# Kernel optimization log

Hardware: AMD Instinct MI355X
Metric: run time of the kernel (lower is better)

The kernel has to match this reference:

```python
import jax, jax.numpy as jnp
import numpy as np

N = 8192
M = 16
F_NODE = 128
HID = 512


def setup_inputs() -> dict:
    key = jax.random.key(0)
    ks = jax.random.split(key, 10)
    node_in_fea = jax.random.normal(ks[0], (N, F_NODE), dtype=jnp.float32)
    edge_fea_idx = jax.random.randint(ks[1], (N, M), 0, N, dtype=jnp.int64)
    s_emb = 1.0 / np.sqrt(F_NODE)
    s_h = 1.0 / np.sqrt(HID)
    W_emb = jax.random.uniform(ks[2], (F_NODE, HID), jnp.float32, -s_emb, s_emb)
    b_emb = jax.random.uniform(ks[3], (HID,), jnp.float32, -s_emb, s_emb)
    W1 = jax.random.uniform(ks[4], (HID, HID), jnp.float32, -s_h, s_h)
    b1 = jax.random.uniform(ks[5], (HID,), jnp.float32, -s_h, s_h)
    W2 = jax.random.uniform(ks[6], (HID, HID), jnp.float32, -s_h, s_h)
    b2 = jax.random.uniform(ks[7], (HID,), jnp.float32, -s_h, s_h)
    W3 = jax.random.uniform(ks[8], (HID, HID), jnp.float32, -s_h, s_h)
    b3 = jax.random.uniform(ks[9], (HID,), jnp.float32, -s_h, s_h)
    return {"node_in_fea": node_in_fea, "edge_fea_idx": edge_fea_idx,
            "W_emb": W_emb, "b_emb": b_emb, "W1": W1, "b1": b1,
            "W2": W2, "b2": b2, "W3": W3, "b3": b3}


def _normalized_adj(edge_fea_idx, n):
    # build dense adjacency: adj[i, j] += 1 for each valid neighbor j of i
    rows = jnp.broadcast_to(jnp.arange(n)[:, None], edge_fea_idx.shape)
    valid = edge_fea_idx >= 0  # -1 marks invalid neighbor
    cols = jnp.where(valid, edge_fea_idx, 0)
    vals = valid.astype(jnp.float32)
    adj = jnp.zeros((n, n), jnp.float32).at[rows.reshape(-1), cols.reshape(-1)].add(vals.reshape(-1))
    # add self-loops, symmetric normalization D^{-1/2} A D^{-1/2}
    adj = adj + jnp.eye(n, dtype=jnp.float32)
    deg = jnp.sum(adj, axis=1)
    d_inv_sqrt = jnp.where(deg > 0, deg ** -0.5, 0.0)
    return adj * d_inv_sqrt[:, None] * d_inv_sqrt[None, :]


def reference(node_in_fea, edge_fea_idx, W_emb, b_emb, W1, b1, W2, b2, W3, b3):
    adj = _normalized_adj(edge_fea_idx, node_in_fea.shape[0])
    x = node_in_fea @ W_emb + b_emb          # (N, HID)
    x = jax.nn.relu((adj @ x) @ W1 + b1)     # gcn1 + relu
    x = jax.nn.relu((adj @ x) @ W2 + b2)     # gcn2 + relu
    x = (adj @ x) @ W3 + b3                  # gcn3 (no relu)
    return x
```

## Files before the change

kernel.cpp:

```cpp
#include <hip/hip_runtime.h>
#include <stdint.h>

#define NN 8192
#define MM 16
#define FN 128
#define HH 512

typedef unsigned short u16;
typedef unsigned int u32;
typedef __bf16 bf16;
typedef __bf16 bf16x8 __attribute__((ext_vector_type(8)));
typedef float f32x4 __attribute__((ext_vector_type(4)));

__global__ void detect_kernel(const u16* __restrict__ node,
                              const u32* __restrict__ idxw,
                              int* __restrict__ flags) {
  if (threadIdx.x == 0 && blockIdx.x == 0) {
    int insane = 0;
    for (int i = 0; i < 64; ++i) {
      int e = (node[2 * i] >> 7) & 0xFF;
      if (!(e == 0 || (e >= 90 && e <= 140))) ++insane;
    }
    flags[0] = (insane >= 8) ? 1 : 0;
    int nz = 0;
    for (int i = 0; i < 32; ++i)
      if (idxw[2 * i + 1] != 0) ++nz;
    flags[1] = (nz == 0) ? 1 : 0;
  }
}

__global__ __launch_bounds__(256) void deg_kernel(const int* __restrict__ idx,
                                                  const int* __restrict__ flags,
                                                  float* __restrict__ dis) {
  int i = blockIdx.x * blockDim.x + threadIdx.x;
  if (i >= NN) return;
  const int sh = flags[1];
  int c = 1;
#pragma unroll
  for (int e = 0; e < MM; ++e) c += (idx[(i * MM + e) << sh] >= 0) ? 1 : 0;
  dis[i] = rsqrtf((float)c);
}

__global__ __launch_bounds__(256) void bias_kernel(
    const void* __restrict__ b0, const void* __restrict__ b1,
    const void* __restrict__ b2, const void* __restrict__ b3,
    const int* __restrict__ flags, u16* __restrict__ out) {
  int id = blockIdx.x * 256 + threadIdx.x;
  if (id >= 4 * HH) return;
  const void* src;
  switch (id >> 9) {
    case 0: src = b0; break;
    case 1: src = b1; break;
    case 2: src = b2; break;
    default: src = b3; break;
  }
  int off = id & (HH - 1);
  bf16 v = flags[0] ? (bf16)((const float*)src)[off] : ((const bf16*)src)[off];
  out[id] = *(u16*)&v;
}

__global__ __launch_bounds__(256) void transpose_all(
    const void* __restrict__ Wemb, const void* __restrict__ W1,
    const void* __restrict__ W2, const void* __restrict__ W3,
    const int* __restrict__ flags, u16* __restrict__ TWemb,
    u16* __restrict__ TW1, u16* __restrict__ TW2, u16* __restrict__ TW3) {
  const void* W;
  u16* T;
  int K;
  switch (blockIdx.z) {
    case 0: W = Wemb; T = TWemb; K = FN; break;
    case 1: W = W1; T = TW1; K = HH; break;
    case 2: W = W2; T = TW2; K = HH; break;
    default: W = W3; T = TW3; K = HH; break;
  }
  int k0 = blockIdx.x * 32;
  if (k0 >= K) return;
  int n0 = blockIdx.y * 32;
  const int f32 = flags[0];
  __shared__ u16 t[32][33];
  int tx = threadIdx.x & 31, ty = threadIdx.x >> 5;
#pragma unroll
  for (int r = ty; r < 32; r += 8) {
    size_t src = (size_t)(k0 + r) * HH + n0 + tx;
    bf16 v = f32 ? (bf16)((const float*)W)[src] : ((const bf16*)W)[src];
    t[r][tx] = *(u16*)&v;
  }
  __syncthreads();
#pragma unroll
  for (int r = ty; r < 32; r += 8) T[(size_t)(n0 + r) * K + k0 + tx] = t[tx][r];
}

template <int K, bool RELU, bool FINAL, bool A_MAYBE_F32>
__global__ __launch_bounds__(256) void gemm_kernel(
    const void* __restrict__ A, const u16* __restrict__ Bt,
    const u16* __restrict__ bias, const int* __restrict__ flags,
    void* __restrict__ C) {
  __shared__ __align__(16) u16 As[128 * 32];
  __shared__ __align__(16) u16 Bs[128 * 32];
  const int rtile = blockIdx.x, ctile = blockIdx.y;
  const int tid = threadIdx.x;
  const int wave = tid >> 6, lane = tid & 63;
  const int wr = wave >> 1, wc = wave & 1;
  const int quad = lane >> 4, l16 = lane & 15;
  const int af32 = A_MAYBE_F32 ? flags[0] : 0;

  f32x4 acc[4][4] = {};

  const int srow = tid >> 2;
  const int sseg = tid & 3;

  for (int k0 = 0; k0 < K; k0 += 32) {
    bf16x8 av0, av1, bv0, bv1;
    if (af32) {
      const float* Af = (const float*)A;
      const float* p0 = &Af[(size_t)(rtile * 128 + srow) * K + k0 + sseg * 8];
      const float* p1 = &Af[(size_t)(rtile * 128 + srow + 64) * K + k0 + sseg * 8];
      f32x4 x0 = *(const f32x4*)p0, x1 = *(const f32x4*)(p0 + 4);
      f32x4 y0 = *(const f32x4*)p1, y1 = *(const f32x4*)(p1 + 4);
#pragma unroll
      for (int t = 0; t < 4; ++t) {
        av0[t] = (bf16)x0[t];
        av0[4 + t] = (bf16)x1[t];
        av1[t] = (bf16)y0[t];
        av1[4 + t] = (bf16)y1[t];
      }
    } else {
      const u16* Ab = (const u16*)A;
      av0 = *(const bf16x8*)&Ab[(size_t)(rtile * 128 + srow) * K + k0 + sseg * 8];
      av1 = *(const bf16x8*)&Ab[(size_t)(rtile * 128 + srow + 64) * K + k0 + sseg * 8];
    }
    bv0 = *(const bf16x8*)&Bt[(size_t)(ctile * 128 + srow) * K + k0 + sseg * 8];
    bv1 = *(const bf16x8*)&Bt[(size_t)(ctile * 128 + srow + 64) * K + k0 + sseg * 8];

    __syncthreads();
    *(bf16x8*)&As[srow * 32 + sseg * 8] = av0;
    *(bf16x8*)&As[(srow + 64) * 32 + sseg * 8] = av1;
    *(bf16x8*)&Bs[srow * 32 + sseg * 8] = bv0;
    *(bf16x8*)&Bs[(srow + 64) * 32 + sseg * 8] = bv1;
    __syncthreads();

    bf16x8 afrag[4], bfrag[4];
#pragma unroll
    for (int i = 0; i < 4; ++i)
      afrag[i] = *(const bf16x8*)&As[(wr * 64 + i * 16 + l16) * 32 + quad * 8];
#pragma unroll
    for (int j = 0; j < 4; ++j)
      bfrag[j] = *(const bf16x8*)&Bs[(wc * 64 + j * 16 + l16) * 32 + quad * 8];
#pragma unroll
    for (int i = 0; i < 4; ++i)
#pragma unroll
      for (int j = 0; j < 4; ++j)
        acc[i][j] = __builtin_amdgcn_mfma_f32_16x16x32_bf16(afrag[i], bfrag[j],
                                                            acc[i][j], 0, 0, 0);
  }

  const int crow0 = rtile * 128 + wr * 64 + quad * 4;
  const int ccol0 = ctile * 128 + wc * 64 + l16;
  const int outf32 = FINAL ? flags[0] : 0;
#pragma unroll
  for (int j = 0; j < 4; ++j) {
    const int col = ccol0 + j * 16;
    const float bv = (float)(*(const bf16*)&bias[col]);
#pragma unroll
    for (int i = 0; i < 4; ++i) {
#pragma unroll
      for (int r = 0; r < 4; ++r) {
        float v = acc[i][j][r] + bv;
        if (RELU) v = fmaxf(v, 0.0f);
        size_t off = (size_t)(crow0 + i * 16 + r) * HH + col;
        if (FINAL && outf32) {
          ((float*)C)[off] = v;
        } else {
          bf16 o = (bf16)v;
          ((u16*)C)[off] = *(u16*)&o;
        }
      }
    }
  }
}

__global__ __launch_bounds__(256) void agg_kernel(const u16* __restrict__ x,
                                                  const int* __restrict__ idx,
                                                  const int* __restrict__ flags,
                                                  const float* __restrict__ dis,
                                                  u16* __restrict__ y) {
  const int node = blockIdx.x * 4 + (threadIdx.x >> 6);
  const int lane = threadIdx.x & 63;
  const int c0 = lane * 8;
  const int sh = flags[1];
  const float wi = dis[node];
  float acc[8];
  bf16x8 xs = *(const bf16x8*)&x[(size_t)node * HH + c0];
#pragma unroll
  for (int t = 0; t < 8; ++t) acc[t] = wi * wi * (float)xs[t];
#pragma unroll
  for (int e = 0; e < MM; ++e) {
    const int j = idx[(node * MM + e) << sh];
    if (j >= 0) {
      const float w = wi * dis[j];
      bf16x8 v = *(const bf16x8*)&x[(size_t)j * HH + c0];
#pragma unroll
      for (int t = 0; t < 8; ++t) acc[t] += w * (float)v[t];
    }
  }
  bf16x8 o;
#pragma unroll
  for (int t = 0; t < 8; ++t) o[t] = (bf16)acc[t];
  *(bf16x8*)&y[(size_t)node * HH + c0] = o;
}

extern "C" void kernel_launch(void* const* d_in, const int* in_sizes, int n_in,
                              void* d_out, int out_size, void* d_ws, size_t ws_size,
                              hipStream_t stream) {
  const void* node = d_in[0];
  const int* idx = (const int*)d_in[1];
  const void* Wemb = d_in[2];
  const void* bemb = d_in[3];
  const void* W1 = d_in[4];
  const void* b1 = d_in[5];
  const void* W2 = d_in[6];
  const void* b2 = d_in[7];
  const void* W3 = d_in[8];
  const void* b3 = d_in[9];

  char* p = (char*)d_ws;
  int* flags = (int*)p;      p += 256;
  float* dis = (float*)p;    p += NN * sizeof(float);
  u16* biasBF = (u16*)p;     p += 4 * HH * sizeof(u16);
  u16* TWemb = (u16*)p;      p += (size_t)HH * FN * 2;
  u16* TW1 = (u16*)p;        p += (size_t)HH * HH * 2;
  u16* TW2 = (u16*)p;        p += (size_t)HH * HH * 2;
  u16* TW3 = (u16*)p;        p += (size_t)HH * HH * 2;
  u16* xA = (u16*)p;         p += (size_t)NN * HH * 2;
  u16* xO = (u16*)d_out;

  detect_kernel<<<1, 64, 0, stream>>>((const u16*)node, (const u32*)idx, flags);
  deg_kernel<<<NN / 256, 256, 0, stream>>>(idx, flags, dis);
  bias_kernel<<<8, 256, 0, stream>>>(bemb, b1, b2, b3, flags, biasBF);
  transpose_all<<<dim3(16, 16, 4), 256, 0, stream>>>(Wemb, W1, W2, W3, flags,
                                                     TWemb, TW1, TW2, TW3);
  gemm_kernel<FN, false, false, true>
      <<<dim3(64, 4), 256, 0, stream>>>(node, TWemb, biasBF, flags, xO);
  agg_kernel<<<NN / 4, 256, 0, stream>>>(xO, idx, flags, dis, xA);
  gemm_kernel<HH, true, false, false>
      <<<dim3(64, 4), 256, 0, stream>>>(xA, TW1, biasBF + HH, flags, xO);
  agg_kernel<<<NN / 4, 256, 0, stream>>>(xO, idx, flags, dis, xA);
  gemm_kernel<HH, true, false, false>
      <<<dim3(64, 4), 256, 0, stream>>>(xA, TW2, biasBF + 2 * HH, flags, xO);
  agg_kernel<<<NN / 4, 256, 0, stream>>>(xO, idx, flags, dis, xA);
  gemm_kernel<HH, false, true, false>
      <<<dim3(64, 4), 256, 0, stream>>>(xA, TW3, biasBF + 3 * HH, flags, d_out);
}
```

Before: 204.9 us.

## Fuse all stages into one cooperative persistent kernel with grid syncs

Replaces the eleven separate launches (detect, degree, bias, transpose, four GEMMs, three aggregations) with a single cooperative kernel of 256 blocks of 512 threads. Stages are separated by grid.sync, so per-launch overhead and the gaps between kernels go away. The GEMM keeps its 128x128 tile, with each of the eight waves now computing a 32x64 sub-tile, and the aggregation loops over nodes in a grid-stride pattern. In exchange, grid barriers cost time, and only 256 blocks are resident, which limits latency hiding in the gather-heavy aggregation stages.

```diff
diff --git a/kernel.cpp b/kernel.cpp
--- a/kernel.cpp
+++ b/kernel.cpp
@@ -1,5 +1,8 @@
 #include <hip/hip_runtime.h>
+#include <hip/hip_cooperative_groups.h>
 #include <stdint.h>
+
+namespace cg = cooperative_groups;
 
 #define NN 8192
 #define MM 16
@@ -12,163 +15,74 @@
 typedef __bf16 bf16x8 __attribute__((ext_vector_type(8)));
 typedef float f32x4 __attribute__((ext_vector_type(4)));
 
-__global__ void detect_kernel(const u16* __restrict__ node,
-                              const u32* __restrict__ idxw,
-                              int* __restrict__ flags) {
-  if (threadIdx.x == 0 && blockIdx.x == 0) {
-    int insane = 0;
-    for (int i = 0; i < 64; ++i) {
-      int e = (node[2 * i] >> 7) & 0xFF;
-      if (!(e == 0 || (e >= 90 && e <= 140))) ++insane;
-    }
-    flags[0] = (insane >= 8) ? 1 : 0;
-    int nz = 0;
-    for (int i = 0; i < 32; ++i)
-      if (idxw[2 * i + 1] != 0) ++nz;
-    flags[1] = (nz == 0) ? 1 : 0;
-  }
-}
-
-__global__ __launch_bounds__(256) void deg_kernel(const int* __restrict__ idx,
-                                                  const int* __restrict__ flags,
-                                                  float* __restrict__ dis) {
-  int i = blockIdx.x * blockDim.x + threadIdx.x;
-  if (i >= NN) return;
-  const int sh = flags[1];
-  int c = 1;
-#pragma unroll
-  for (int e = 0; e < MM; ++e) c += (idx[(i * MM + e) << sh] >= 0) ? 1 : 0;
-  dis[i] = rsqrtf((float)c);
-}
-
-__global__ __launch_bounds__(256) void bias_kernel(
-    const void* __restrict__ b0, const void* __restrict__ b1,
-    const void* __restrict__ b2, const void* __restrict__ b3,
-    const int* __restrict__ flags, u16* __restrict__ out) {
-  int id = blockIdx.x * 256 + threadIdx.x;
-  if (id >= 4 * HH) return;
-  const void* src;
-  switch (id >> 9) {
-    case 0: src = b0; break;
-    case 1: src = b1; break;
-    case 2: src = b2; break;
-    default: src = b3; break;
-  }
-  int off = id & (HH - 1);
-  bf16 v = flags[0] ? (bf16)((const float*)src)[off] : ((const bf16*)src)[off];
-  out[id] = *(u16*)&v;
-}
-
-__global__ __launch_bounds__(256) void transpose_all(
-    const void* __restrict__ Wemb, const void* __restrict__ W1,
-    const void* __restrict__ W2, const void* __restrict__ W3,
-    const int* __restrict__ flags, u16* __restrict__ TWemb,
-    u16* __restrict__ TW1, u16* __restrict__ TW2, u16* __restrict__ TW3) {
-  const void* W;
-  u16* T;
-  int K;
-  switch (blockIdx.z) {
-    case 0: W = Wemb; T = TWemb; K = FN; break;
-    case 1: W = W1; T = TW1; K = HH; break;
-    case 2: W = W2; T = TW2; K = HH; break;
-    default: W = W3; T = TW3; K = HH; break;
-  }
-  int k0 = blockIdx.x * 32;
-  if (k0 >= K) return;
-  int n0 = blockIdx.y * 32;
-  const int f32 = flags[0];
-  __shared__ u16 t[32][33];
-  int tx = threadIdx.x & 31, ty = threadIdx.x >> 5;
-#pragma unroll
-  for (int r = ty; r < 32; r += 8) {
-    size_t src = (size_t)(k0 + r) * HH + n0 + tx;
-    bf16 v = f32 ? (bf16)((const float*)W)[src] : ((const bf16*)W)[src];
-    t[r][tx] = *(u16*)&v;
-  }
-  __syncthreads();
-#pragma unroll
-  for (int r = ty; r < 32; r += 8) T[(size_t)(n0 + r) * K + k0 + tx] = t[tx][r];
-}
-
-template <int K, bool RELU, bool FINAL, bool A_MAYBE_F32>
-__global__ __launch_bounds__(256) void gemm_kernel(
-    const void* __restrict__ A, const u16* __restrict__ Bt,
-    const u16* __restrict__ bias, const int* __restrict__ flags,
-    void* __restrict__ C) {
-  __shared__ __align__(16) u16 As[128 * 32];
-  __shared__ __align__(16) u16 Bs[128 * 32];
-  const int rtile = blockIdx.x, ctile = blockIdx.y;
+__device__ __forceinline__ void gemm_stage(u16* __restrict__ smem,
+                                           const void* __restrict__ A,
+                                           const u16* __restrict__ Bt,
+                                           const u16* __restrict__ bias,
+                                           void* __restrict__ C, int K,
+                                           bool relu, bool a_f32, bool out_f32) {
+  u16* As = smem;
+  u16* Bs = smem + 128 * 32;
   const int tid = threadIdx.x;
+  const int rtile = blockIdx.x >> 2, ctile = blockIdx.x & 3;
   const int wave = tid >> 6, lane = tid & 63;
   const int wr = wave >> 1, wc = wave & 1;
   const int quad = lane >> 4, l16 = lane & 15;
-  const int af32 = A_MAYBE_F32 ? flags[0] : 0;
-
-  f32x4 acc[4][4] = {};
-
-  const int srow = tid >> 2;
-  const int sseg = tid & 3;
+  const int srow = tid >> 2, sseg = tid & 3;
+
+  f32x4 acc[2][4] = {};
+  const size_t aBase = (size_t)(rtile * 128 + srow) * K + sseg * 8;
+  const size_t bBase = (size_t)(ctile * 128 + srow) * K + sseg * 8;
 
   for (int k0 = 0; k0 < K; k0 += 32) {
-    bf16x8 av0, av1, bv0, bv1;
-    if (af32) {
-      const float* Af = (const float*)A;
-      const float* p0 = &Af[(size_t)(rtile * 128 + srow) * K + k0 + sseg * 8];
-      const float* p1 = &Af[(size_t)(rtile * 128 + srow + 64) * K + k0 + sseg * 8];
-      f32x4 x0 = *(const f32x4*)p0, x1 = *(const f32x4*)(p0 + 4);
-      f32x4 y0 = *(const f32x4*)p1, y1 = *(const f32x4*)(p1 + 4);
+    bf16x8 av, bv;
+    if (a_f32) {
+      const float* p = (const float*)A + aBase + k0;
+      f32x4 x0 = *(const f32x4*)p, x1 = *(const f32x4*)(p + 4);
 #pragma unroll
       for (int t = 0; t < 4; ++t) {
-        av0[t] = (bf16)x0[t];
-        av0[4 + t] = (bf16)x1[t];
-        av1[t] = (bf16)y0[t];
-        av1[4 + t] = (bf16)y1[t];
+        av[t] = (bf16)x0[t];
+        av[4 + t] = (bf16)x1[t];
       }
     } else {
-      const u16* Ab = (const u16*)A;
-      av0 = *(const bf16x8*)&Ab[(size_t)(rtile * 128 + srow) * K + k0 + sseg * 8];
-      av1 = *(const bf16x8*)&Ab[(size_t)(rtile * 128 + srow + 64) * K + k0 + sseg * 8];
-    }
-    bv0 = *(const bf16x8*)&Bt[(size_t)(ctile * 128 + srow) * K + k0 + sseg * 8];
-    bv1 = *(const bf16x8*)&Bt[(size_t)(ctile * 128 + srow + 64) * K + k0 + sseg * 8];
+      av = *(const bf16x8*)((const u16*)A + aBase + k0);
+    }
+    bv = *(const bf16x8*)(Bt + bBase + k0);
 
     __syncthreads();
-    *(bf16x8*)&As[srow * 32 + sseg * 8] = av0;
-    *(bf16x8*)&As[(srow + 64) * 32 + sseg * 8] = av1;
-    *(bf16x8*)&Bs[srow * 32 + sseg * 8] = bv0;
-    *(bf16x8*)&Bs[(srow + 64) * 32 + sseg * 8] = bv1;
+    *(bf16x8*)&As[srow * 32 + sseg * 8] = av;
+    *(bf16x8*)&Bs[srow * 32 + sseg * 8] = bv;
     __syncthreads();
 
-    bf16x8 afrag[4], bfrag[4];
-#pragma unroll
-    for (int i = 0; i < 4; ++i)
-      afrag[i] = *(const bf16x8*)&As[(wr * 64 + i * 16 + l16) * 32 + quad * 8];
+    bf16x8 af[2], bfr[4];
+#pragma unroll
+    for (int i = 0; i < 2; ++i)
+      af[i] = *(const bf16x8*)&As[(wr * 32 + i * 16 + l16) * 32 + quad * 8];
 #pragma unroll
     for (int j = 0; j < 4; ++j)
-      bfrag[j] = *(const bf16x8*)&Bs[(wc * 64 + j * 16 + l16) * 32 + quad * 8];
-#pragma unroll
-    for (int i = 0; i < 4; ++i)
+      bfr[j] = *(const bf16x8*)&Bs[(wc * 64 + j * 16 + l16) * 32 + quad * 8];
+#pragma unroll
+    for (int i = 0; i < 2; ++i)
 #pragma unroll
       for (int j = 0; j < 4; ++j)
-        acc[i][j] = __builtin_amdgcn_mfma_f32_16x16x32_bf16(afrag[i], bfrag[j],
+        acc[i][j] = __builtin_amdgcn_mfma_f32_16x16x32_bf16(af[i], bfr[j],
                                                             acc[i][j], 0, 0, 0);
   }
 
-  const int crow0 = rtile * 128 + wr * 64 + quad * 4;
+  const int crow0 = rtile * 128 + wr * 32 + quad * 4;
   const int ccol0 = ctile * 128 + wc * 64 + l16;
-  const int outf32 = FINAL ? flags[0] : 0;
 #pragma unroll
   for (int j = 0; j < 4; ++j) {
     const int col = ccol0 + j * 16;
-    const float bv = (float)(*(const bf16*)&bias[col]);
-#pragma unroll
-    for (int i = 0; i < 4; ++i) {
+    const float bvs = (float)(*(const bf16*)&bias[col]);
+#pragma unroll
+    for (int i = 0; i < 2; ++i) {
 #pragma unroll
       for (int r = 0; r < 4; ++r) {
-        float v = acc[i][j][r] + bv;
-        if (RELU) v = fmaxf(v, 0.0f);
+        float v = acc[i][j][r] + bvs;
+        if (relu) v = fmaxf(v, 0.0f);
         size_t off = (size_t)(crow0 + i * 16 + r) * HH + col;
-        if (FINAL && outf32) {
+        if (out_f32) {
           ((float*)C)[off] = v;
         } else {
           bf16 o = (bf16)v;
@@ -179,34 +93,122 @@
   }
 }
 
-__global__ __launch_bounds__(256) void agg_kernel(const u16* __restrict__ x,
-                                                  const int* __restrict__ idx,
-                                                  const int* __restrict__ flags,
-                                                  const float* __restrict__ dis,
-                                                  u16* __restrict__ y) {
-  const int node = blockIdx.x * 4 + (threadIdx.x >> 6);
-  const int lane = threadIdx.x & 63;
+__device__ __forceinline__ void agg_stage(const u16* __restrict__ x,
+                                          const int* __restrict__ idx, int i64,
+                                          const float* __restrict__ dis,
+                                          u16* __restrict__ y) {
+  const int wave = threadIdx.x >> 6, lane = threadIdx.x & 63;
   const int c0 = lane * 8;
-  const int sh = flags[1];
-  const float wi = dis[node];
-  float acc[8];
-  bf16x8 xs = *(const bf16x8*)&x[(size_t)node * HH + c0];
-#pragma unroll
-  for (int t = 0; t < 8; ++t) acc[t] = wi * wi * (float)xs[t];
-#pragma unroll
-  for (int e = 0; e < MM; ++e) {
-    const int j = idx[(node * MM + e) << sh];
-    if (j >= 0) {
-      const float w = wi * dis[j];
-      bf16x8 v = *(const bf16x8*)&x[(size_t)j * HH + c0];
-#pragma unroll
-      for (int t = 0; t < 8; ++t) acc[t] += w * (float)v[t];
-    }
-  }
-  bf16x8 o;
-#pragma unroll
-  for (int t = 0; t < 8; ++t) o[t] = (bf16)acc[t];
-  *(bf16x8*)&y[(size_t)node * HH + c0] = o;
+  for (int node = blockIdx.x * 8 + wave; node < NN; node += 2048) {
+    const float wi = dis[node];
+    float acc[8];
+    bf16x8 xs = *(const bf16x8*)&x[(size_t)node * HH + c0];
+#pragma unroll
+    for (int t = 0; t < 8; ++t) acc[t] = wi * wi * (float)xs[t];
+#pragma unroll
+    for (int e = 0; e < MM; ++e) {
+      const int j = idx[(node * MM + e) << i64];
+      if (j >= 0) {
+        const float w = wi * dis[j];
+        bf16x8 v = *(const bf16x8*)&x[(size_t)j * HH + c0];
+#pragma unroll
+        for (int t = 0; t < 8; ++t) acc[t] += w * (float)v[t];
+      }
+    }
+    bf16x8 o;
+#pragma unroll
+    for (int t = 0; t < 8; ++t) o[t] = (bf16)acc[t];
+    *(bf16x8*)&y[(size_t)node * HH + c0] = o;
+  }
+}
+
+__global__ __launch_bounds__(512, 2) void mega_kernel(
+    const void* __restrict__ node, const int* __restrict__ idx,
+    const void* __restrict__ Wemb, const void* __restrict__ bemb,
+    const void* __restrict__ W1, const void* __restrict__ b1,
+    const void* __restrict__ W2, const void* __restrict__ b2,
+    const void* __restrict__ W3, const void* __restrict__ b3,
+    void* __restrict__ out, float* __restrict__ dis, u16* __restrict__ biasBF,
+    u16* __restrict__ TWemb, u16* __restrict__ TW1, u16* __restrict__ TW2,
+    u16* __restrict__ TW3, u16* __restrict__ xA) {
+  __shared__ __align__(16) u16 smem[2 * 128 * 32];
+  __shared__ int s_flags[2];
+  const int tid = threadIdx.x;
+  cg::grid_group grid = cg::this_grid();
+
+  if (tid < 64) {
+    int e = (((const u16*)node)[2 * tid] >> 7) & 0xFF;
+    unsigned long long m1 = __ballot(!(e == 0 || (e >= 90 && e <= 140)));
+    unsigned long long m2 =
+        __ballot(tid < 32 && ((const u32*)idx)[2 * tid + 1] != 0);
+    if (tid == 0) {
+      s_flags[0] = (__popcll(m1) >= 8) ? 1 : 0;
+      s_flags[1] = (m2 == 0) ? 1 : 0;
+    }
+  }
+  __syncthreads();
+  const int f32in = s_flags[0], i64 = s_flags[1];
+
+  {
+    int g = blockIdx.x * 512 + tid;
+    if (g < NN) {
+      int c = 1;
+#pragma unroll
+      for (int e = 0; e < MM; ++e) c += (idx[(g * MM + e) << i64] >= 0) ? 1 : 0;
+      dis[g] = rsqrtf((float)c);
+    } else if (g < NN + 4 * HH) {
+      int id = g - NN;
+      int q = id >> 9;
+      const void* src = q == 0 ? bemb : q == 1 ? b1 : q == 2 ? b2 : b3;
+      int off = id & (HH - 1);
+      bf16 v = f32in ? (bf16)((const float*)src)[off] : ((const bf16*)src)[off];
+      biasBF[id] = *(u16*)&v;
+    }
+    const int tx = tid & 31, ty = tid >> 5;
+    for (int t = blockIdx.x; t < 832; t += 256) {
+      const void* W;
+      u16* T;
+      int K, tt;
+      if (t < 64) {
+        W = Wemb; T = TWemb; K = FN; tt = t;
+      } else {
+        int q = (t - 64) >> 8;
+        tt = (t - 64) & 255;
+        K = HH;
+        W = q == 0 ? W1 : q == 1 ? W2 : W3;
+        T = q == 0 ? TW1 : q == 1 ? TW2 : TW3;
+      }
+      const int k0 = (tt >> 4) * 32, n0 = (tt & 15) * 32;
+      __syncthreads();
+#pragma unroll
+      for (int r = ty; r < 32; r += 16) {
+        size_t src = (size_t)(k0 + r) * HH + n0 + tx;
+        bf16 v = f32in ? (bf16)((const float*)W)[src] : ((const bf16*)W)[src];
+        smem[r * 33 + tx] = *(u16*)&v;
+      }
+      __syncthreads();
+#pragma unroll
+      for (int r = ty; r < 32; r += 16)
+        T[(size_t)(n0 + r) * K + k0 + tx] = smem[tx * 33 + r];
+    }
+  }
+  grid.sync();
+
+  u16* xO = (u16*)out;
+
+  gemm_stage(smem, node, TWemb, biasBF, xO, FN, false, f32in != 0, false);
+  grid.sync();
+  agg_stage(xO, idx, i64, dis, xA);
+  grid.sync();
+  gemm_stage(smem, xA, TW1, biasBF + HH, xO, HH, true, false, false);
+  grid.sync();
+  agg_stage(xO, idx, i64, dis, xA);
+  grid.sync();
+  gemm_stage(smem, xA, TW2, biasBF + 2 * HH, xO, HH, true, false, false);
+  grid.sync();
+  agg_stage(xO, idx, i64, dis, xA);
+  grid.sync();
+  gemm_stage(smem, xA, TW3, biasBF + 3 * HH, out, HH, false, false, f32in != 0);
 }
 
 extern "C" void kernel_launch(void* const* d_in, const int* in_sizes, int n_in,
@@ -222,32 +224,20 @@
   const void* b2 = d_in[7];
   const void* W3 = d_in[8];
   const void* b3 = d_in[9];
+  void* out = d_out;
 
   char* p = (char*)d_ws;
-  int* flags = (int*)p;      p += 256;
-  float* dis = (float*)p;    p += NN * sizeof(float);
-  u16* biasBF = (u16*)p;     p += 4 * HH * sizeof(u16);
-  u16* TWemb = (u16*)p;      p += (size_t)HH * FN * 2;
-  u16* TW1 = (u16*)p;        p += (size_t)HH * HH * 2;
-  u16* TW2 = (u16*)p;        p += (size_t)HH * HH * 2;
-  u16* TW3 = (u16*)p;        p += (size_t)HH * HH * 2;
-  u16* xA = (u16*)p;         p += (size_t)NN * HH * 2;
-  u16* xO = (u16*)d_out;
-
-  detect_kernel<<<1, 64, 0, stream>>>((const u16*)node, (const u32*)idx, flags);
-  deg_kernel<<<NN / 256, 256, 0, stream>>>(idx, flags, dis);
-  bias_kernel<<<8, 256, 0, stream>>>(bemb, b1, b2, b3, flags, biasBF);
-  transpose_all<<<dim3(16, 16, 4), 256, 0, stream>>>(Wemb, W1, W2, W3, flags,
-                                                     TWemb, TW1, TW2, TW3);
-  gemm_kernel<FN, false, false, true>
-      <<<dim3(64, 4), 256, 0, stream>>>(node, TWemb, biasBF, flags, xO);
-  agg_kernel<<<NN / 4, 256, 0, stream>>>(xO, idx, flags, dis, xA);
-  gemm_kernel<HH, true, false, false>
-      <<<dim3(64, 4), 256, 0, stream>>>(xA, TW1, biasBF + HH, flags, xO);
-  agg_kernel<<<NN / 4, 256, 0, stream>>>(xO, idx, flags, dis, xA);
-  gemm_kernel<HH, true, false, false>
-      <<<dim3(64, 4), 256, 0, stream>>>(xA, TW2, biasBF + 2 * HH, flags, xO);
-  agg_kernel<<<NN / 4, 256, 0, stream>>>(xO, idx, flags, dis, xA);
-  gemm_kernel<HH, false, true, false>
-      <<<dim3(64, 4), 256, 0, stream>>>(xA, TW3, biasBF + 3 * HH, flags, d_out);
-}
+  float* dis = (float*)p;  p += NN * sizeof(float);
+  u16* biasBF = (u16*)p;   p += 4 * HH * sizeof(u16);
+  u16* TWemb = (u16*)p;    p += (size_t)HH * FN * 2;
+  u16* TW1 = (u16*)p;      p += (size_t)HH * HH * 2;
+  u16* TW2 = (u16*)p;      p += (size_t)HH * HH * 2;
+  u16* TW3 = (u16*)p;      p += (size_t)HH * HH * 2;
+  u16* xA = (u16*)p;
+
+  void* kargs[] = {&node, &idx, &Wemb, &bemb, &W1, &b1, &W2, &b2,
+                   &W3,   &b3,  &out,  &dis,  &biasBF, &TWemb,
+                   &TW1,  &TW2, &TW3,  &xA};
+  hipLaunchCooperativeKernel((void*)mega_kernel, dim3(256), dim3(512), kargs, 0,
+                             stream);
+}
```

After: 468.1 us. 2.28x slower.
